# Kernel tuning notes

Hardware: AMD Instinct MI355X
Metric: run time of the kernel (lower is better)

## Reference

```python
import jax, jax.numpy as jnp
import numpy as np

B, CIN, H, W = 16, 32, 32, 32
OC, K = 64, 3
ALPHA = 0.0005625
VD = 0.1
DENOM = 2 * 1.5 * 0.025  # 2*n*VT
V_MIN, V_MAX = 0.0, 9.0
TH_MIN, TH_MAX = 1.0, 8.0


def setup_inputs() -> dict:
    key = jax.random.key(0)
    kx, kt = jax.random.split(key)
    x = jax.random.uniform(kx, (B, CIN, H, W), dtype=jnp.float32)
    # theta drawn in [TH_MIN, TH_MAX] so the in-forward clamp is an identity
    theta = jax.random.uniform(kt, (OC, CIN, K, K), dtype=jnp.float32,
                               minval=TH_MIN, maxval=TH_MAX)
    return {"x": x, "theta": theta}


def _ekv_f(v, t):
    # f(V, theta) = log(1 + exp(clip((V - theta)/denom, -50, 50)))**2
    arg = jnp.clip((v - t) / DENOM, -50.0, 50.0)
    return jnp.log1p(jnp.exp(arg)) ** 2


def reference(x, theta):
    theta_c = jnp.clip(theta, TH_MIN, TH_MAX)
    x_c = jnp.clip(x, V_MIN, V_MAX)
    # im2col: [B, CIN*K*K, Ho, Wo]; feature dim ordered (c, kh, kw) like torch unfold
    patches = jax.lax.conv_general_dilated_patches(
        x_c, filter_shape=(K, K), window_strides=(1, 1),
        padding=[(1, 1), (1, 1)])
    b, ckk, ho, wo = patches.shape
    vg = patches.reshape(b, ckk, ho * wo).transpose(0, 2, 1)  # [B, L, CKK]
    th = theta_c.reshape(OC, ckk)                              # [OC, CKK]
    # broadcast nonlinearity over output channels, reduce over patch dim
    vg4 = vg[:, :, None, :]          # [B, L, 1, CKK]
    th4 = th[None, None, :, :]       # [1, 1, OC, CKK]
    ik = ALPHA * jnp.sum(_ekv_f(vg4, th4) - _ekv_f(vg4, th4 + VD), axis=-1)  # [B, L, OC]
    return ik.transpose(0, 2, 1).reshape(b, OC, ho, wo)
```

## Files before the change

kernel.cpp:

```cpp
#include <hip/hip_runtime.h>


#define B_    16
#define CIN_  32
#define H_    32
#define W_    32
#define OC_   64
#define CKK_  288

#define INV_D  13.333333333333334f
#define ALPHA_ 0.0005625f
#define KC     0.26359713811572677f
#define C2_    0.93051654475128f
#define C3_    0.98168436111127f
#define C4_    0.91224137800000f

#define WS_VMAX   0
#define WS_CNTA   256
#define WS_CNTB   512
#define WS_LISTA  1024
#define WS_LISTB  (1024 + 64*288*8)
#define WS_NEEDED (WS_LISTB + 64*288*8)

__device__ __forceinline__ float clipf(float v, float lo, float hi) {
    return fminf(fmaxf(v, lo), hi);
}

__global__ void vmax_kernel(const float4* __restrict__ x4, unsigned* __restrict__ vmax, int n4) {
    float m = 0.0f;
    for (int i = blockIdx.x * blockDim.x + threadIdx.x; i < n4; i += gridDim.x * blockDim.x) {
        float4 v = x4[i];
        m = fmaxf(fmaxf(m, clipf(v.x, 0.0f, 9.0f)),
                  fmaxf(clipf(v.y, 0.0f, 9.0f),
                        fmaxf(clipf(v.z, 0.0f, 9.0f), clipf(v.w, 0.0f, 9.0f))));
    }
    #pragma unroll
    for (int off = 32; off > 0; off >>= 1)
        m = fmaxf(m, __shfl_down(m, off, 64));
    __shared__ float sm[4];
    int lane = threadIdx.x & 63, wid = threadIdx.x >> 6;
    if (lane == 0) sm[wid] = m;
    __syncthreads();
    if (threadIdx.x == 0) {
        float mm = fmaxf(fmaxf(sm[0], sm[1]), fmaxf(sm[2], sm[3]));
        atomicMax(vmax, __float_as_uint(mm));
    }
}

__global__ void build_lists(const float* __restrict__ theta,
                            const unsigned* __restrict__ vmax_u,
                            int* __restrict__ cntA, int* __restrict__ cntB,
                            int2* __restrict__ listA, int2* __restrict__ listB) {
    __shared__ int sA, sB;
    if (threadIdx.x == 0) { sA = 0; sB = 0; }
    __syncthreads();
    const int oc = blockIdx.x;
    const float vmax = __uint_as_float(*vmax_u);
    const float cutB = vmax + 0.6f;
    const float cutA = vmax + 0.131f;
    for (int j = threadIdx.x; j < CKK_; j += blockDim.x) {
        float t = clipf(theta[oc * CKK_ + j], 1.0f, 8.0f);
        if (t < cutB) {
            int cin = j / 9;
            int r   = j - cin * 9;
            int2 e;
            e.x = cin * 136 + (r / 3) * 34 + (r % 3);
            e.y = __float_as_int(__expf(-t * INV_D));
            if (t < cutA) { int i = atomicAdd(&sA, 1); listA[oc * CKK_ + i] = e; }
            else          { int i = atomicAdd(&sB, 1); listB[oc * CKK_ + i] = e; }
        }
    }
    __syncthreads();
    if (threadIdx.x == 0) { cntA[oc] = sA; cntB[oc] = sB; }
}

__launch_bounds__(256, 4)
__global__ void nlmain(const float* __restrict__ x,
                       const int* __restrict__ cntA, const int* __restrict__ cntB,
                       const int2* __restrict__ listA, const int2* __restrict__ listB,
                       float* __restrict__ out) {
    __shared__ float sx[CIN_ * 136];

    const int blk = blockIdx.x;
    const int ocg = blk & 3;
    const int rp  = (blk >> 2) & 15;
    const int b   = blk >> 6;

    for (int idx = threadIdx.x; idx < CIN_ * 136; idx += 256) {
        int cin = idx / 136;
        int rem = idx - cin * 136;
        int rr  = rem / 34;
        int cc  = rem - rr * 34;
        int ir  = rp * 2 - 1 + rr;
        int ic  = cc - 1;
        float ev = 1.0f;
        if ((unsigned)ir < (unsigned)H_ && (unsigned)ic < (unsigned)W_)
            ev = __expf(clipf(x[((b * CIN_ + cin) * H_ + ir) * W_ + ic], 0.0f, 9.0f) * INV_D);
        sx[idx] = ev;
    }
    __syncthreads();

    const int lane = threadIdx.x & 63;
    const int wv   = threadIdx.x >> 6;
    const int rl   = lane >> 5;
    const int w    = lane & 31;
    const int myoff = rl * 34 + w;
    const int row  = rp * 2 + rl;

    const int ocbase = __builtin_amdgcn_readfirstlane(ocg * 16 + wv * 4);

    #pragma unroll
    for (int k = 0; k < 4; ++k) {
        const int oc = ocbase + k;
        const int ca = cntA[oc];
        const int cb = cntB[oc];
        const int2* __restrict__ LA = listA + oc * CKK_;
        const int2* __restrict__ LB = listB + oc * CKK_;

        float accA = 0.0f, accB = 0.0f;

        #pragma unroll 2
        for (int i = 0; i < ca; ++i) {
            const int2 e  = LA[i];
            const float u = sx[e.x + myoff] * __int_as_float(e.y);
            const float l1 = __logf(1.0f + u);
            const float l2 = __logf(fmaf(u, KC, 1.0f));
            accA += (l1 - l2) * (l1 + l2);
        }
        #pragma unroll 4
        for (int i = 0; i < cb; ++i) {
            const int2 e  = LB[i];
            const float u = sx[e.x + myoff] * __int_as_float(e.y);
            float p = fmaf(u, C4_, -C3_);
            p = fmaf(u, p, C2_);
            accB = fmaf(u * u, p, accB);
        }

        out[((b * OC_ + oc) * H_ + row) * W_ + w] = ALPHA_ * (accA + accB);
    }
}

__launch_bounds__(256)
__global__ void nlconv_fallback(const float* __restrict__ x,
                                const float* __restrict__ theta,
                                float* __restrict__ out,
                                const unsigned* __restrict__ vmax_u) {
    __shared__ int   s_base[CKK_];
    __shared__ float s_t[CKK_];
    __shared__ int   s_d[CKK_];
    __shared__ int   s_cnt;
    const int blk = blockIdx.x;
    const int b  = blk >> 6;
    const int oc = blk & 63;
    if (threadIdx.x == 0) s_cnt = 0;
    __syncthreads();
    const float vmax   = __uint_as_float(*vmax_u);
    const float cutoff = vmax + 0.6f;
    for (int j = threadIdx.x; j < CKK_; j += blockDim.x) {
        float t = clipf(theta[oc * CKK_ + j], 1.0f, 8.0f);
        if (t < cutoff) {
            int i = atomicAdd(&s_cnt, 1);
            int cin = j / 9;
            int r   = j - cin * 9;
            s_base[i] = cin * (H_ * W_);
            s_t[i]    = t;
            s_d[i]    = (r / 3) | ((r % 3) << 8);
        }
    }
    __syncthreads();
    const int cnt = s_cnt;
    const float* xb = x + b * (CIN_ * H_ * W_);
    const int w  = threadIdx.x & 31;
    const int h0 = threadIdx.x >> 5;
    float acc[4] = {0.f, 0.f, 0.f, 0.f};
    for (int i = 0; i < cnt; ++i) {
        const float t    = s_t[i];
        const int   base = s_base[i];
        const int   d    = s_d[i];
        const int   rdh  = (d & 0xff) - 1;
        const int   rdw  = (d >> 8) - 1;
        const int  col   = w + rdw;
        const bool colok = (unsigned)col < (unsigned)W_;
        const int  ccol  = min(max(col, 0), W_ - 1);
        const float tq   = t * INV_D;
        #pragma unroll
        for (int k = 0; k < 4; ++k) {
            const int  row   = h0 + k * 8 + rdh;
            const bool rowok = (unsigned)row < (unsigned)H_;
            const int  crow  = min(max(row, 0), H_ - 1);
            const float xv   = xb[base + crow * W_ + ccol];
            const float v    = (rowok && colok) ? clipf(xv, 0.0f, 9.0f) : 0.0f;
            const float arg  = fmaf(v, INV_D, -tq);
            const float e1   = __expf(arg);
            const float e2   = e1 * KC;
            const float l1   = __logf(1.0f + e1);
            const float l2   = __logf(1.0f + e2);
            acc[k] += (l1 - l2) * (l1 + l2);
        }
    }
    float* ob = out + (b * OC_ + oc) * (H_ * W_);
    #pragma unroll
    for (int k = 0; k < 4; ++k)
        ob[(h0 + k * 8) * W_ + w] = ALPHA_ * acc[k];
}

extern "C" void kernel_launch(void* const* d_in, const int* in_sizes, int n_in,
                              void* d_out, int out_size, void* d_ws, size_t ws_size,
                              hipStream_t stream) {
    const float* x     = (const float*)d_in[0];
    const float* theta = (const float*)d_in[1];
    float* out = (float*)d_out;
    char* ws = (char*)d_ws;

    unsigned* vmax = (unsigned*)(ws + WS_VMAX);
    hipMemsetAsync(vmax, 0, sizeof(unsigned), stream);

    const int n4 = (B_ * CIN_ * H_ * W_) / 4;
    vmax_kernel<<<64, 256, 0, stream>>>((const float4*)x, vmax, n4);

    if (ws_size >= (size_t)WS_NEEDED) {
        int*  cntA  = (int*)(ws + WS_CNTA);
        int*  cntB  = (int*)(ws + WS_CNTB);
        int2* listA = (int2*)(ws + WS_LISTA);
        int2* listB = (int2*)(ws + WS_LISTB);

        build_lists<<<OC_, 128, 0, stream>>>(theta, vmax, cntA, cntB, listA, listB);
        nlmain<<<B_ * 16 * 4, 256, 0, stream>>>(x, cntA, cntB, listA, listB, out);
    } else {
        nlconv_fallback<<<B_ * OC_, 256, 0, stream>>>(x, theta, out, vmax);
    }
}
```

Before: 81.12 us.

## Precompute exp(x) once in prep kernel, drop memset, vectorize tile loads

The vmax pass now also writes exp(clip(x)/D) into a workspace buffer, so nlmain loads precomputed values with float4 reads into a padded shared tile instead of recomputing exp and doing scalar index math per element. The atomicMax plus memset is replaced by per-block partial maxima that build_lists reduces itself, which removes one launch and the atomic. This adds a 2 MB workspace write and read in exchange for fewer exps and fewer integer ops in the main kernel. The fallback now uses a fixed cutoff.

```diff
diff --git a/kernel.cpp b/kernel.cpp
--- a/kernel.cpp
+++ b/kernel.cpp
@@ -15,47 +15,67 @@
 #define C3_    0.98168436111127f
 #define C4_    0.91224137800000f
 
-#define WS_VMAX   0
-#define WS_CNTA   256
-#define WS_CNTB   512
-#define WS_LISTA  1024
-#define WS_LISTB  (1024 + 64*288*8)
-#define WS_NEEDED (WS_LISTB + 64*288*8)
+#define TSTR   40
+#define TSTRC  (4 * TSTR)
+#define TWORDS (CIN_ * TSTRC)
+
+#define WS_EV     0
+#define WS_PART   2097152
+#define WS_CNTA   2097664
+#define WS_CNTB   2097920
+#define WS_LISTA  2098176
+#define WS_LISTB  (WS_LISTA + OC_*CKK_*8)
+#define WS_NEEDED (WS_LISTB + OC_*CKK_*8)
 
 __device__ __forceinline__ float clipf(float v, float lo, float hi) {
     return fminf(fmaxf(v, lo), hi);
 }
 
-__global__ void vmax_kernel(const float4* __restrict__ x4, unsigned* __restrict__ vmax, int n4) {
+__global__ void prep(const float4* __restrict__ x4, float4* __restrict__ ev4,
+                     float* __restrict__ part, int n4) {
     float m = 0.0f;
-    for (int i = blockIdx.x * blockDim.x + threadIdx.x; i < n4; i += gridDim.x * blockDim.x) {
+    for (int i = blockIdx.x * blockDim.x + threadIdx.x; i < n4;
+         i += gridDim.x * blockDim.x) {
         float4 v = x4[i];
-        m = fmaxf(fmaxf(m, clipf(v.x, 0.0f, 9.0f)),
-                  fmaxf(clipf(v.y, 0.0f, 9.0f),
-                        fmaxf(clipf(v.z, 0.0f, 9.0f), clipf(v.w, 0.0f, 9.0f))));
+        float a = clipf(v.x, 0.0f, 9.0f);
+        float b = clipf(v.y, 0.0f, 9.0f);
+        float c = clipf(v.z, 0.0f, 9.0f);
+        float d = clipf(v.w, 0.0f, 9.0f);
+        m = fmaxf(m, fmaxf(fmaxf(a, b), fmaxf(c, d)));
+        float4 e;
+        e.x = __expf(a * INV_D);
+        e.y = __expf(b * INV_D);
+        e.z = __expf(c * INV_D);
+        e.w = __expf(d * INV_D);
+        ev4[i] = e;
     }
     #pragma unroll
     for (int off = 32; off > 0; off >>= 1)
         m = fmaxf(m, __shfl_down(m, off, 64));
     __shared__ float sm[4];
-    int lane = threadIdx.x & 63, wid = threadIdx.x >> 6;
+    const int lane = threadIdx.x & 63, wid = threadIdx.x >> 6;
     if (lane == 0) sm[wid] = m;
     __syncthreads();
-    if (threadIdx.x == 0) {
-        float mm = fmaxf(fmaxf(sm[0], sm[1]), fmaxf(sm[2], sm[3]));
-        atomicMax(vmax, __float_as_uint(mm));
-    }
+    if (threadIdx.x == 0)
+        part[blockIdx.x] = fmaxf(fmaxf(sm[0], sm[1]), fmaxf(sm[2], sm[3]));
 }
 
 __global__ void build_lists(const float* __restrict__ theta,
-                            const unsigned* __restrict__ vmax_u,
+                            const float* __restrict__ part,
                             int* __restrict__ cntA, int* __restrict__ cntB,
                             int2* __restrict__ listA, int2* __restrict__ listB) {
+    __shared__ float svmax;
     __shared__ int sA, sB;
     if (threadIdx.x == 0) { sA = 0; sB = 0; }
-    __syncthreads();
+    float m = (threadIdx.x < 64) ? part[threadIdx.x] : 0.0f;
+    #pragma unroll
+    for (int off = 32; off > 0; off >>= 1)
+        m = fmaxf(m, __shfl_down(m, off, 64));
+    if (threadIdx.x == 0) svmax = m;
+    __syncthreads();
+
     const int oc = blockIdx.x;
-    const float vmax = __uint_as_float(*vmax_u);
+    const float vmax = svmax;
     const float cutB = vmax + 0.6f;
     const float cutA = vmax + 0.131f;
     for (int j = threadIdx.x; j < CKK_; j += blockDim.x) {
@@ -64,7 +84,7 @@
             int cin = j / 9;
             int r   = j - cin * 9;
             int2 e;
-            e.x = cin * 136 + (r / 3) * 34 + (r % 3);
+            e.x = cin * TSTRC + (r / 3) * TSTR + 3 + (r % 3);
             e.y = __float_as_int(__expf(-t * INV_D));
             if (t < cutA) { int i = atomicAdd(&sA, 1); listA[oc * CKK_ + i] = e; }
             else          { int i = atomicAdd(&sB, 1); listB[oc * CKK_ + i] = e; }
@@ -75,28 +95,35 @@
 }
 
 __launch_bounds__(256, 4)
-__global__ void nlmain(const float* __restrict__ x,
+__global__ void nlmain(const float* __restrict__ ev,
                        const int* __restrict__ cntA, const int* __restrict__ cntB,
                        const int2* __restrict__ listA, const int2* __restrict__ listB,
                        float* __restrict__ out) {
-    __shared__ float sx[CIN_ * 136];
+    __shared__ float sx[TWORDS];
 
     const int blk = blockIdx.x;
     const int ocg = blk & 3;
     const int rp  = (blk >> 2) & 15;
     const int b   = blk >> 6;
 
-    for (int idx = threadIdx.x; idx < CIN_ * 136; idx += 256) {
-        int cin = idx / 136;
-        int rem = idx - cin * 136;
-        int rr  = rem / 34;
-        int cc  = rem - rr * 34;
-        int ir  = rp * 2 - 1 + rr;
-        int ic  = cc - 1;
-        float ev = 1.0f;
-        if ((unsigned)ir < (unsigned)H_ && (unsigned)ic < (unsigned)W_)
-            ev = __expf(clipf(x[((b * CIN_ + cin) * H_ + ir) * W_ + ic], 0.0f, 9.0f) * INV_D);
-        sx[idx] = ev;
+    {
+        const float4* evb = (const float4*)(ev) + b * (CIN_ * H_ * W_ / 4);
+        const int c4 = threadIdx.x & 7;
+        const int r0 = threadIdx.x >> 3;
+        #pragma unroll
+        for (int s = 0; s < 4; ++s) {
+            const int rowIdx = r0 + s * 32;
+            const int cin = rowIdx >> 2;
+            const int rr  = rowIdx & 3;
+            const int ir  = rp * 2 - 1 + rr;
+            float4 v = make_float4(1.0f, 1.0f, 1.0f, 1.0f);
+            if ((unsigned)ir < (unsigned)H_)
+                v = evb[(cin * H_ + ir) * (W_ / 4) + c4];
+            *(float4*)&sx[rowIdx * TSTR + 4 + c4 * 4] = v;
+        }
+        const int hrow = threadIdx.x & 127;
+        const int side = threadIdx.x >> 7;
+        sx[hrow * TSTR + 3 + side * 33] = 1.0f;
     }
     __syncthreads();
 
@@ -104,7 +131,7 @@
     const int wv   = threadIdx.x >> 6;
     const int rl   = lane >> 5;
     const int w    = lane & 31;
-    const int myoff = rl * 34 + w;
+    const int myoff = rl * TSTR + w;
     const int row  = rp * 2 + rl;
 
     const int ocbase = __builtin_amdgcn_readfirstlane(ocg * 16 + wv * 4);
@@ -143,8 +170,7 @@
 __launch_bounds__(256)
 __global__ void nlconv_fallback(const float* __restrict__ x,
                                 const float* __restrict__ theta,
-                                float* __restrict__ out,
-                                const unsigned* __restrict__ vmax_u) {
+                                float* __restrict__ out) {
     __shared__ int   s_base[CKK_];
     __shared__ float s_t[CKK_];
     __shared__ int   s_d[CKK_];
@@ -154,8 +180,7 @@
     const int oc = blk & 63;
     if (threadIdx.x == 0) s_cnt = 0;
     __syncthreads();
-    const float vmax   = __uint_as_float(*vmax_u);
-    const float cutoff = vmax + 0.6f;
+    const float cutoff = 9.6f;
     for (int j = threadIdx.x; j < CKK_; j += blockDim.x) {
         float t = clipf(theta[oc * CKK_ + j], 1.0f, 8.0f);
         if (t < cutoff) {
@@ -212,21 +237,19 @@
     float* out = (float*)d_out;
     char* ws = (char*)d_ws;
 
-    unsigned* vmax = (unsigned*)(ws + WS_VMAX);
-    hipMemsetAsync(vmax, 0, sizeof(unsigned), stream);
-
-    const int n4 = (B_ * CIN_ * H_ * W_) / 4;
-    vmax_kernel<<<64, 256, 0, stream>>>((const float4*)x, vmax, n4);
-
     if (ws_size >= (size_t)WS_NEEDED) {
-        int*  cntA  = (int*)(ws + WS_CNTA);
-        int*  cntB  = (int*)(ws + WS_CNTB);
-        int2* listA = (int2*)(ws + WS_LISTA);
-        int2* listB = (int2*)(ws + WS_LISTB);
-
-        build_lists<<<OC_, 128, 0, stream>>>(theta, vmax, cntA, cntB, listA, listB);
-        nlmain<<<B_ * 16 * 4, 256, 0, stream>>>(x, cntA, cntB, listA, listB, out);
+        float* evbuf = (float*)(ws + WS_EV);
+        float* part  = (float*)(ws + WS_PART);
+        int*  cntA   = (int*)(ws + WS_CNTA);
+        int*  cntB   = (int*)(ws + WS_CNTB);
+        int2* listA  = (int2*)(ws + WS_LISTA);
+        int2* listB  = (int2*)(ws + WS_LISTB);
+
+        const int n4 = (B_ * CIN_ * H_ * W_) / 4;
+        prep<<<64, 256, 0, stream>>>((const float4*)x, (float4*)evbuf, part, n4);
+        build_lists<<<OC_, 128, 0, stream>>>(theta, part, cntA, cntB, listA, listB);
+        nlmain<<<B_ * 16 * 4, 256, 0, stream>>>(evbuf, cntA, cntB, listA, listB, out);
     } else {
-        nlconv_fallback<<<B_ * OC_, 256, 0, stream>>>(x, theta, out, vmax);
-    }
-}
+        nlconv_fallback<<<B_ * OC_, 256, 0, stream>>>(x, theta, out);
+    }
+}
```

New measurement: 76.78 us. 5.4% less time.
